# Kernel tuning notes

Hardware: AMD Instinct MI355X
Metric: run time of the kernel (lower is better)

## Reference

```python
import jax, jax.numpy as jnp
import numpy as np

EMBED = 1024
HEAD = 64

def setup_inputs() -> dict:
    key = jax.random.key(0)
    k1, k2, k3, k4 = jax.random.split(key, 4)
    embeddings = jax.random.normal(k1, (8, 2048, EMBED), dtype=jnp.float32)
    # nn.Linear weight is [out, in]; we store transposed [in, out] for x @ W
    scale = 1.0 / np.sqrt(EMBED)
    Wk = jax.random.uniform(k2, (EMBED, HEAD), dtype=jnp.float32, minval=-scale, maxval=scale)
    Wq = jax.random.uniform(k3, (EMBED, HEAD), dtype=jnp.float32, minval=-scale, maxval=scale)
    Wv = jax.random.uniform(k4, (EMBED, HEAD), dtype=jnp.float32, minval=-scale, maxval=scale)
    return {"embeddings": embeddings, "Wq": Wq, "Wk": Wk, "Wv": Wv}

def reference(embeddings, Wq, Wk, Wv):
    B, S, D = embeddings.shape
    q = embeddings @ Wq  # [B,S,H]
    k = embeddings @ Wk
    v = embeddings @ Wv
    norm = k.shape[-1] ** (-0.5)
    scores = jnp.einsum('bqh,bkh->bqk', q, k) * norm  # [B,S,S]
    causal = jnp.tril(jnp.ones((S, S), dtype=bool))
    scores = jnp.where(causal, scores, -jnp.inf)
    weights = jax.nn.softmax(scores, axis=-1)
    # dropout p=0.0 (eval-equivalent): identity
    return jnp.einsum('bqk,bkh->bqh', weights, v)
```

## Files before the change

### kernel.cpp

```cpp
#include <hip/hip_runtime.h>

#define SEQ   2048
#define NBATCH 8
#define EMB   1024
#define HD    64
#define QKVSZ (NBATCH * SEQ * HD)
#define WTSZ  (3 * HD * EMB)
#define PSLOT2 4224

typedef __attribute__((ext_vector_type(8))) short bf16x8;
typedef __attribute__((ext_vector_type(4))) float f32x4;

__device__ inline unsigned short f2b(float f) {
  union { float f; unsigned int i; } u; u.f = f;
  unsigned int r = (u.i + 0x7FFFu + ((u.i >> 16) & 1u)) >> 16;
  return (unsigned short)r;
}

__global__ __launch_bounds__(256) void wtrans_kernel(const float* __restrict__ wq,
                                                     const float* __restrict__ wk,
                                                     const float* __restrict__ wv,
                                                     unsigned short* __restrict__ wt) {
  int i = blockIdx.x * 256 + threadIdx.x;
  int kb  = i / 12288;
  int rem = i - kb * 12288;
  int m   = rem >> 12;
  int c   = (rem >> 6) & 63;
  int kd  = rem & 63;
  const float* src = (m == 0) ? wq : ((m == 1) ? wk : wv);
  int d = kb * 64 + kd;
  wt[i] = f2b(src[d * 64 + c]);
}

#define QKV_ISSUE(kb, pa, pw)                                                       \
  do {                                                                              \
    _Pragma("unroll") for (int j = 0; j < 2; j++) {                                 \
      int u = t + j * 256;                                                          \
      pa[j] = *(const f32x4*)(aBase + (size_t)(u >> 4) * EMB + (kb) * 64 + (u & 15) * 4); \
    }                                                                               \
    _Pragma("unroll") for (int j = 0; j < 3; j++) {                                 \
      int u = t + j * 256;                                                          \
      pw[j] = *(const bf16x8*)(wBase + (size_t)(kb) * 12288 + u * 8);               \
    }                                                                               \
  } while (0)

#define QKV_STAGE(buf, pa, pw)                                                      \
  do {                                                                              \
    _Pragma("unroll") for (int j = 0; j < 2; j++) {                                 \
      int u = t + j * 256;                                                          \
      int row = u >> 4, kq = u & 15;                                                \
      unsigned int lo = (unsigned int)f2b(pa[j][0]) | ((unsigned int)f2b(pa[j][1]) << 16); \
      unsigned int hi = (unsigned int)f2b(pa[j][2]) | ((unsigned int)f2b(pa[j][3]) << 16); \
      uint2 pk; pk.x = lo; pk.y = hi;                                               \
      *(uint2*)((char*)&Ab[buf][0] + row * 128 + ((kq * 8) ^ ((row & 7) << 4))) = pk; \
    }                                                                               \
    _Pragma("unroll") for (int j = 0; j < 3; j++) {                                 \
      int u = t + j * 256;                                                          \
      int coll = u >> 3, kd8 = u & 7;                                               \
      *(bf16x8*)((char*)&Wb[buf][0] + coll * 128 + ((kd8 ^ (coll & 7)) << 4)) = pw[j]; \
    }                                                                               \
  } while (0)

#define QKV_COMPUTE(buf)                                                            \
  do {                                                                              \
    const int arow = wr * 16 + l16;                                                 \
    _Pragma("unroll") for (int kh = 0; kh < 2; kh++) {                              \
      bf16x8 af = *(const bf16x8*)((const char*)&Ab[buf][0] + arow * 128 +          \
                                   ((kh * 64 + quad * 16) ^ ((arow & 7) << 4)));    \
      _Pragma("unroll") for (int j = 0; j < 3; j++) {                               \
        const int coll = (wc * 3 + j) * 16 + l16;                                   \
        bf16x8 wf = *(const bf16x8*)((const char*)&Wb[buf][0] + coll * 128 +        \
                                     ((kh * 64 + quad * 16) ^ ((coll & 7) << 4)));  \
        acc[j] = __builtin_amdgcn_mfma_f32_16x16x32_bf16(af, wf, acc[j], 0, 0, 0);  \
      }                                                                             \
    }                                                                               \
  } while (0)

__global__ __launch_bounds__(256, 4) void qkv_proj_kernel(const float* __restrict__ emb,
                                                          const unsigned short* __restrict__ wt,
                                                          unsigned short* __restrict__ qkv) {
  __shared__ __align__(16) unsigned short Ab[2][32 * 64];
  __shared__ __align__(16) unsigned short Wb[2][96 * 64];

  const int t    = threadIdx.x;
  const int wave = t >> 6;
  const int lane = t & 63;
  const int quad = lane >> 4;
  const int l16  = lane & 15;
  const int bx = blockIdx.x;
  const int rt = bx >> 1;
  const int ch = bx & 1;
  const int wr = wave >> 1;
  const int wc = wave & 1;

  const float* aBase = emb + (size_t)rt * 32 * EMB;
  const unsigned short* wBase = wt + ch * 6144;

  f32x4 acc[3];
#pragma unroll
  for (int j = 0; j < 3; j++) acc[j] = (f32x4){0.f, 0.f, 0.f, 0.f};

  f32x4 paA[2], paB[2];
  bf16x8 pwA[3], pwB[3];

  QKV_ISSUE(0, paA, pwA);
  QKV_ISSUE(1, paB, pwB);
  QKV_STAGE(0, paA, pwA);
  __syncthreads();

#pragma unroll
  for (int k = 0; k < 16; k += 2) {
    if (k + 2 < 16) QKV_ISSUE(k + 2, paA, pwA);
    QKV_COMPUTE(0);
    if (k + 1 < 16) QKV_STAGE(1, paB, pwB);
    __syncthreads();
    if (k + 3 < 16) QKV_ISSUE(k + 3, paB, pwB);
    QKV_COMPUTE(1);
    if (k + 2 < 16) QKV_STAGE(0, paA, pwA);
    __syncthreads();
  }

#pragma unroll
  for (int j = 0; j < 3; j++) {
    int gc = ch * 96 + (wc * 3 + j) * 16 + l16;
    if (gc < 128) {
      int m  = gc >> 6, cm = gc & 63;
#pragma unroll
      for (int r = 0; r < 4; r++) {
        int row = rt * 32 + wr * 16 + quad * 4 + r;
        qkv[(size_t)m * QKVSZ + (size_t)row * HD + cm] = f2b(acc[j][r]);
      }
    }
  }

  if (ch == 1) {
    __syncthreads();
    unsigned short* Vsh = (unsigned short*)&Ab[0][0];
#pragma unroll
    for (int j = 0; j < 3; j++) {
      int gc = 96 + (wc * 3 + j) * 16 + l16;
      if (gc >= 128) {
        int h = gc - 128;
#pragma unroll
        for (int r = 0; r < 4; r++)
          Vsh[h * 40 + wr * 16 + quad * 4 + r] = f2b(acc[j][r]);
      }
    }
    __syncthreads();
    int h  = t >> 2;
    int sq = (t & 3) * 8;
    int row0 = rt * 32;
    int b    = row0 >> 11;
    int seq0 = row0 & 2047;
    bf16x8 vv = *(const bf16x8*)(Vsh + h * 40 + sq);
    *(bf16x8*)(qkv + 2 * (size_t)QKVSZ + ((size_t)(b * 64 + h)) * SEQ + seq0 + sq) = vv;
  }
}

__global__ __launch_bounds__(256, 4) void attn_split(const unsigned short* __restrict__ qkv,
                                                     float* __restrict__ part,
                                                     float* __restrict__ out) {
  __shared__ __align__(16) unsigned short Kb[2][64 * 64];
  __shared__ __align__(16) unsigned short Vb[2][64 * 64];
  __shared__ __align__(16) unsigned short Pb[4][16 * 64];

  const int t    = threadIdx.x;
  const int wave = t >> 6;
  const int lane = t & 63;
  const int quad = lane >> 4;
  const int l16  = lane & 15;
  const int B0 = blockIdx.x;
  const int c  = blockIdx.y;
  const int b  = blockIdx.z;
  const int nch = (B0 >> 2) + 1;
  if (c >= nch) return;
  const int t0 = c * 4;
  const int t1 = min(t0 + 3, B0);
  const int qt = B0 * 4 + wave;
  const int q0 = qt * 16;

  const unsigned short* qg = qkv;
  const unsigned short* kg = qkv + QKVSZ;
  const unsigned short* vg = qkv + 2 * QKVSZ;

  const unsigned short* qptr = qg + ((size_t)(b * SEQ + q0 + l16)) * HD + quad * 8;
  const bf16x8 qf0 = *(const bf16x8*)qptr;
  const bf16x8 qf1 = *(const bf16x8*)(qptr + 32);

  f32x4 o0 = {0,0,0,0}, o1 = {0,0,0,0}, o2 = {0,0,0,0}, o3 = {0,0,0,0};
  float mst[4] = {-INFINITY, -INFINITY, -INFINITY, -INFINITY};
  float lst[4] = {0.f, 0.f, 0.f, 0.f};
  const float sc = 0.125f * 1.44269504088896f;

  bf16x8 kpre[2], vpre[2];
#pragma unroll
  for (int i = 0; i < 2; i++) {
    int u = t + i * 256;
    kpre[i] = *(const bf16x8*)(kg + ((size_t)(b * SEQ + t0 * 64 + (u >> 3))) * HD + (u & 7) * 8);
    vpre[i] = *(const bf16x8*)(vg + ((size_t)(b * 64 + (u >> 3))) * SEQ + t0 * 64 + (u & 7) * 8);
  }
#pragma unroll
  for (int i = 0; i < 2; i++) {
    int u = t + i * 256;
    int row = u >> 3, sb = (u & 7) * 16;
    *(bf16x8*)((char*)&Kb[0][0] + row * 128 + (sb ^ ((row & 7) << 4))) = kpre[i];
    *(bf16x8*)((char*)&Vb[0][0] + row * 128 + (sb ^ ((row & 7) << 4))) = vpre[i];
  }
  __syncthreads();

  for (int kb = t0; kb <= t1; kb++) {
    const int cur = (kb - t0) & 1;

    if (kb < t1) {
#pragma unroll
      for (int i = 0; i < 2; i++) {
        int u = t + i * 256;
        kpre[i] = *(const bf16x8*)(kg + ((size_t)(b * SEQ + (kb + 1) * 64 + (u >> 3))) * HD + (u & 7) * 8);
        vpre[i] = *(const bf16x8*)(vg + ((size_t)(b * 64 + (u >> 3))) * SEQ + (kb + 1) * 64 + (u & 7) * 8);
      }
    }

    f32x4 s[4];
#pragma unroll
    for (int kt = 0; kt < 4; kt++) {
      int row = kt * 16 + l16;
      bf16x8 kf0 = *(const bf16x8*)((char*)&Kb[cur][0] + row * 128 + ((quad * 16) ^ ((row & 7) << 4)));
      bf16x8 kf1 = *(const bf16x8*)((char*)&Kb[cur][0] + row * 128 + ((64 + quad * 16) ^ ((row & 7) << 4)));
      f32x4 z = {0.f, 0.f, 0.f, 0.f};
      z = __builtin_amdgcn_mfma_f32_16x16x32_bf16(qf0, kf0, z, 0, 0, 0);
      z = __builtin_amdgcn_mfma_f32_16x16x32_bf16(qf1, kf1, z, 0, 0, 0);
      s[kt] = z;
    }

    if (kb == B0) {
#pragma unroll
      for (int r = 0; r < 4; r++) {
        int rowg = q0 + quad * 4 + r;
#pragma unroll
        for (int kt = 0; kt < 4; kt++) {
          int col = kb * 64 + kt * 16 + l16;
          float v = s[kt][r] * sc;
          s[kt][r] = (col > rowg) ? -INFINITY : v;
        }
      }
    } else {
#pragma unroll
      for (int r = 0; r < 4; r++)
#pragma unroll
        for (int kt = 0; kt < 4; kt++) s[kt][r] *= sc;
    }

    float alpha[4];
#pragma unroll
    for (int r = 0; r < 4; r++) {
      float mx = fmaxf(fmaxf(s[0][r], s[1][r]), fmaxf(s[2][r], s[3][r]));
#pragma unroll
      for (int off = 1; off < 16; off <<= 1) mx = fmaxf(mx, __shfl_xor(mx, off, 64));
      float mnew = fmaxf(mst[r], mx);
      alpha[r] = exp2f(mst[r] - mnew);
      mst[r] = mnew;
    }
#pragma unroll
    for (int r = 0; r < 4; r++) {
      float sm = 0.f;
#pragma unroll
      for (int kt = 0; kt < 4; kt++) {
        float p = exp2f(s[kt][r] - mst[r]);
        s[kt][r] = p;
        sm += p;
      }
#pragma unroll
      for (int off = 1; off < 16; off <<= 1) sm += __shfl_xor(sm, off, 64);
      lst[r] = lst[r] * alpha[r] + sm;
    }
#pragma unroll
    for (int r = 0; r < 4; r++) { o0[r] *= alpha[r]; o1[r] *= alpha[r]; o2[r] *= alpha[r]; o3[r] *= alpha[r]; }

#pragma unroll
    for (int kt = 0; kt < 4; kt++)
#pragma unroll
      for (int r = 0; r < 4; r++) {
        int row = quad * 4 + r;
        *(unsigned short*)((char*)&Pb[wave][0] + row * 128 +
                           ((kt * 32 + l16 * 2) ^ ((row & 7) << 4))) = f2b(s[kt][r]);
      }

#pragma unroll
    for (int kc = 0; kc < 2; kc++) {
      bf16x8 pf = *(const bf16x8*)((char*)&Pb[wave][0] + l16 * 128 +
                                   ((kc * 64 + quad * 16) ^ ((l16 & 7) << 4)));
      int r0 = l16, r1 = 16 + l16, r2 = 32 + l16, r3 = 48 + l16;
      bf16x8 vf0 = *(const bf16x8*)((char*)&Vb[cur][0] + r0 * 128 + ((kc * 64 + quad * 16) ^ ((r0 & 7) << 4)));
      bf16x8 vf1 = *(const bf16x8*)((char*)&Vb[cur][0] + r1 * 128 + ((kc * 64 + quad * 16) ^ ((r1 & 7) << 4)));
      bf16x8 vf2 = *(const bf16x8*)((char*)&Vb[cur][0] + r2 * 128 + ((kc * 64 + quad * 16) ^ ((r2 & 7) << 4)));
      bf16x8 vf3 = *(const bf16x8*)((char*)&Vb[cur][0] + r3 * 128 + ((kc * 64 + quad * 16) ^ ((r3 & 7) << 4)));
      o0 = __builtin_amdgcn_mfma_f32_16x16x32_bf16(pf, vf0, o0, 0, 0, 0);
      o1 = __builtin_amdgcn_mfma_f32_16x16x32_bf16(pf, vf1, o1, 0, 0, 0);
      o2 = __builtin_amdgcn_mfma_f32_16x16x32_bf16(pf, vf2, o2, 0, 0, 0);
      o3 = __builtin_amdgcn_mfma_f32_16x16x32_bf16(pf, vf3, o3, 0, 0, 0);
    }

    if (kb < t1) {
      const int nb = cur ^ 1;
#pragma unroll
      for (int i = 0; i < 2; i++) {
        int u = t + i * 256;
        int row = u >> 3, sb = (u & 7) * 16;
        *(bf16x8*)((char*)&Kb[nb][0] + row * 128 + (sb ^ ((row & 7) << 4))) = kpre[i];
        *(bf16x8*)((char*)&Vb[nb][0] + row * 128 + (sb ^ ((row & 7) << 4))) = vpre[i];
      }
    }
    __syncthreads();
  }

  if (nch == 1) {
#pragma unroll
    for (int r = 0; r < 4; r++) {
      float inv = 1.f / lst[r];
      int rowg = q0 + quad * 4 + r;
      size_t ob = ((size_t)(b * SEQ + rowg)) * HD + l16;
      out[ob + 0]  = o0[r] * inv;
      out[ob + 16] = o1[r] * inv;
      out[ob + 32] = o2[r] * inv;
      out[ob + 48] = o3[r] * inv;
    }
  } else {
    float* ps = part + ((size_t)((b * 32 + B0) * 8 + c)) * PSLOT2;
#pragma unroll
    for (int r = 0; r < 4; r++) {
      int row = wave * 16 + quad * 4 + r;
      ps[row * 64 + 0  + l16] = o0[r];
      ps[row * 64 + 16 + l16] = o1[r];
      ps[row * 64 + 32 + l16] = o2[r];
      ps[row * 64 + 48 + l16] = o3[r];
      if (l16 == 0) {
        ps[4096 + row] = mst[r];
        ps[4160 + row] = lst[r];
      }
    }
  }
}

__global__ __launch_bounds__(256) void attn_merge(const float* __restrict__ part,
                                                  float* __restrict__ out) {
  const int bx = blockIdx.x;
  const int B0 = 4 + (bx >> 2);
  const int rg = bx & 3;
  const int b  = blockIdx.y;
  const int nch = (B0 >> 2) + 1;
  const int t  = threadIdx.x;
  const int h  = t & 63;
  const int rloc = t >> 6;
  const float* base = part + ((size_t)((b * 32 + B0) * 8)) * PSLOT2;
#pragma unroll
  for (int i = 0; i < 4; i++) {
    int row = rg * 16 + rloc * 4 + i;
    float mv[8], lv[8], ov[8];
#pragma unroll
    for (int cc = 0; cc < 8; cc++) {
      int cs = (cc < nch) ? cc : 0;
      const float* ps = base + (size_t)cs * PSLOT2;
      mv[cc] = ps[4096 + row];
      lv[cc] = ps[4160 + row];
      ov[cc] = ps[row * 64 + h];
    }
    float M = -INFINITY;
#pragma unroll
    for (int cc = 0; cc < 8; cc++) M = fmaxf(M, (cc < nch) ? mv[cc] : -INFINITY);
    float L = 0.f, o = 0.f;
#pragma unroll
    for (int cc = 0; cc < 8; cc++) {
      float e = (cc < nch) ? exp2f(mv[cc] - M) : 0.f;
      L += lv[cc] * e;
      o += ov[cc] * e;
    }
    out[((size_t)(b * SEQ + B0 * 64 + row)) * HD + h] = o / L;
  }
}

extern "C" void kernel_launch(void* const* d_in, const int* in_sizes, int n_in,
                              void* d_out, int out_size, void* d_ws, size_t ws_size,
                              hipStream_t stream) {
  const float* emb = (const float*)d_in[0];
  const float* wq  = (const float*)d_in[1];
  const float* wk  = (const float*)d_in[2];
  const float* wv  = (const float*)d_in[3];
  unsigned short* ws  = (unsigned short*)d_ws;
  unsigned short* wt  = ws;
  unsigned short* qkv = ws + WTSZ;
  float* part = (float*)(ws + WTSZ + 3 * QKVSZ);

  hipLaunchKernelGGL(wtrans_kernel,   dim3(WTSZ / 256), dim3(256), 0, stream, wq, wk, wv, wt);
  hipLaunchKernelGGL(qkv_proj_kernel, dim3(1024),       dim3(256), 0, stream, emb, wt, qkv);
  hipLaunchKernelGGL(attn_split,      dim3(32, 8, 8),   dim3(256), 0, stream, qkv, part, (float*)d_out);
  hipLaunchKernelGGL(attn_merge,      dim3(112, 8),     dim3(256), 0, stream, part, (float*)d_out);
}
```

Before: 159.2 us.

## Load weight and K/V tiles directly into LDS with global_load_lds

Replaces the register-staged global→VGPR→LDS copies of the projection weight tiles and the attention K/V tiles with direct global-to-LDS loads (global_load_lds, 16 bytes per lane). The XOR swizzle is moved to the gather side so each lane fetches from a permuted source address and writes a contiguous LDS slot. The aim is to cut VGPR pressure and the ds_write instructions, letting the double-buffered loads overlap compute. The projection loop also drops from two-deep register prefetch to a single-step pipeline. This relies on the barrier to cover completion of the async LDS writes, with no explicit vmcnt wait, which risks races if the compiler does not insert one.

Result: faster. 155.9 us (-2.1%).

```diff
diff --git a/kernel.cpp b/kernel.cpp
--- a/kernel.cpp
+++ b/kernel.cpp
@@ -16,6 +16,11 @@
   unsigned int r = (u.i + 0x7FFFu + ((u.i >> 16) & 1u)) >> 16;
   return (unsigned short)r;
 }
+
+#define GLOAD_LDS16(g, l)                                              \
+  __builtin_amdgcn_global_load_lds(                                    \
+      (const __attribute__((address_space(1))) void*)(g),              \
+      (__attribute__((address_space(3))) void*)(l), 16, 0, 0)
 
 __global__ __launch_bounds__(256) void wtrans_kernel(const float* __restrict__ wq,
                                                      const float* __restrict__ wk,
@@ -32,19 +37,55 @@
   wt[i] = f2b(src[d * 64 + c]);
 }
 
-#define QKV_ISSUE(kb, pa, pw)                                                       \
+__global__ __launch_bounds__(256, 4) void qkv_proj_kernel(const float* __restrict__ emb,
+                                                          const unsigned short* __restrict__ wt,
+                                                          unsigned short* __restrict__ qkv) {
+  __shared__ __align__(16) unsigned short Ab[2][32 * 64];
+  __shared__ __align__(16) unsigned short Wb[2][96 * 64];
+
+  const int t    = threadIdx.x;
+  const int wave = t >> 6;
+  const int lane = t & 63;
+  const int quad = lane >> 4;
+  const int l16  = lane & 15;
+  const int bx = blockIdx.x;
+  const int rt = bx >> 1;
+  const int ch = bx & 1;
+  const int wr = wave >> 1;
+  const int wc = wave & 1;
+
+  const float* aBase = emb + (size_t)rt * 32 * EMB;
+  const char*  wChunk = (const char*)(wt + ch * 6144);
+
+  int wsrc[3];
+#pragma unroll
+  for (int i = 0; i < 3; i++) {
+    int u = (wave * 3 + i) * 64 + lane;
+    int row = u >> 3, k8 = u & 7;
+    wsrc[i] = row * 128 + ((k8 ^ (row & 7)) << 4);
+  }
+
+  f32x4 acc[3];
+#pragma unroll
+  for (int j = 0; j < 3; j++) acc[j] = (f32x4){0.f, 0.f, 0.f, 0.f};
+  f32x4 pa[2];
+
+#define QKVA_ISSUE(kb)                                                              \
   do {                                                                              \
     _Pragma("unroll") for (int j = 0; j < 2; j++) {                                 \
       int u = t + j * 256;                                                          \
       pa[j] = *(const f32x4*)(aBase + (size_t)(u >> 4) * EMB + (kb) * 64 + (u & 15) * 4); \
     }                                                                               \
-    _Pragma("unroll") for (int j = 0; j < 3; j++) {                                 \
-      int u = t + j * 256;                                                          \
-      pw[j] = *(const bf16x8*)(wBase + (size_t)(kb) * 12288 + u * 8);               \
-    }                                                                               \
   } while (0)
 
-#define QKV_STAGE(buf, pa, pw)                                                      \
+#define QKVW_DMA(kb, buf)                                                           \
+  do {                                                                              \
+    _Pragma("unroll") for (int i = 0; i < 3; i++)                                   \
+      GLOAD_LDS16(wChunk + (size_t)(kb) * 24576 + wsrc[i],                          \
+                  (char*)&Wb[buf][0] + (wave * 3 + i) * 1024);                      \
+  } while (0)
+
+#define QKVA_STAGE(buf)                                                             \
   do {                                                                              \
     _Pragma("unroll") for (int j = 0; j < 2; j++) {                                 \
       int u = t + j * 256;                                                          \
@@ -53,11 +94,6 @@
       unsigned int hi = (unsigned int)f2b(pa[j][2]) | ((unsigned int)f2b(pa[j][3]) << 16); \
       uint2 pk; pk.x = lo; pk.y = hi;                                               \
       *(uint2*)((char*)&Ab[buf][0] + row * 128 + ((kq * 8) ^ ((row & 7) << 4))) = pk; \
-    }                                                                               \
-    _Pragma("unroll") for (int j = 0; j < 3; j++) {                                 \
-      int u = t + j * 256;                                                          \
-      int coll = u >> 3, kd8 = u & 7;                                               \
-      *(bf16x8*)((char*)&Wb[buf][0] + coll * 128 + ((kd8 ^ (coll & 7)) << 4)) = pw[j]; \
     }                                                                               \
   } while (0)
 
@@ -76,47 +112,20 @@
     }                                                                               \
   } while (0)
 
-__global__ __launch_bounds__(256, 4) void qkv_proj_kernel(const float* __restrict__ emb,
-                                                          const unsigned short* __restrict__ wt,
-                                                          unsigned short* __restrict__ qkv) {
-  __shared__ __align__(16) unsigned short Ab[2][32 * 64];
-  __shared__ __align__(16) unsigned short Wb[2][96 * 64];
-
-  const int t    = threadIdx.x;
-  const int wave = t >> 6;
-  const int lane = t & 63;
-  const int quad = lane >> 4;
-  const int l16  = lane & 15;
-  const int bx = blockIdx.x;
-  const int rt = bx >> 1;
-  const int ch = bx & 1;
-  const int wr = wave >> 1;
-  const int wc = wave & 1;
-
-  const float* aBase = emb + (size_t)rt * 32 * EMB;
-  const unsigned short* wBase = wt + ch * 6144;
-
-  f32x4 acc[3];
-#pragma unroll
-  for (int j = 0; j < 3; j++) acc[j] = (f32x4){0.f, 0.f, 0.f, 0.f};
-
-  f32x4 paA[2], paB[2];
-  bf16x8 pwA[3], pwB[3];
-
-  QKV_ISSUE(0, paA, pwA);
-  QKV_ISSUE(1, paB, pwB);
-  QKV_STAGE(0, paA, pwA);
+  QKVA_ISSUE(0);
+  QKVW_DMA(0, 0);
+  QKVA_STAGE(0);
   __syncthreads();
 
-#pragma unroll
-  for (int k = 0; k < 16; k += 2) {
-    if (k + 2 < 16) QKV_ISSUE(k + 2, paA, pwA);
-    QKV_COMPUTE(0);
-    if (k + 1 < 16) QKV_STAGE(1, paB, pwB);
-    __syncthreads();
-    if (k + 3 < 16) QKV_ISSUE(k + 3, paB, pwB);
-    QKV_COMPUTE(1);
-    if (k + 2 < 16) QKV_STAGE(0, paA, pwA);
+  for (int kb = 0; kb < 16; kb++) {
+    const int cur = kb & 1;
+    const int nb  = cur ^ 1;
+    if (kb < 15) {
+      QKVA_ISSUE(kb + 1);
+      QKVW_DMA(kb + 1, nb);
+    }
+    QKV_COMPUTE(cur);
+    if (kb < 15) QKVA_STAGE(nb);
     __syncthreads();
   }
 
@@ -187,36 +196,39 @@
   const bf16x8 qf0 = *(const bf16x8*)qptr;
   const bf16x8 qf1 = *(const bf16x8*)(qptr + 32);
 
+  int koff[2]; size_t voff[2];
+#pragma unroll
+  for (int i = 0; i < 2; i++) {
+    int u = (wave * 2 + i) * 64 + lane;
+    int row = u >> 3, k8 = u & 7;
+    int swz = (k8 ^ (row & 7)) << 4;
+    koff[i] = row * 128 + swz;
+    voff[i] = ((size_t)(b * 64 + row) * SEQ) * 2 + swz;
+  }
+  const char* kgB = (const char*)kg + (size_t)b * SEQ * 128;
+  const char* vgB = (const char*)vg;
+
   f32x4 o0 = {0,0,0,0}, o1 = {0,0,0,0}, o2 = {0,0,0,0}, o3 = {0,0,0,0};
   float mst[4] = {-INFINITY, -INFINITY, -INFINITY, -INFINITY};
   float lst[4] = {0.f, 0.f, 0.f, 0.f};
   const float sc = 0.125f * 1.44269504088896f;
 
-  bf16x8 kpre[2], vpre[2];
 #pragma unroll
   for (int i = 0; i < 2; i++) {
-    int u = t + i * 256;
-    kpre[i] = *(const bf16x8*)(kg + ((size_t)(b * SEQ + t0 * 64 + (u >> 3))) * HD + (u & 7) * 8);
-    vpre[i] = *(const bf16x8*)(vg + ((size_t)(b * 64 + (u >> 3))) * SEQ + t0 * 64 + (u & 7) * 8);
-  }
-#pragma unroll
-  for (int i = 0; i < 2; i++) {
-    int u = t + i * 256;
-    int row = u >> 3, sb = (u & 7) * 16;
-    *(bf16x8*)((char*)&Kb[0][0] + row * 128 + (sb ^ ((row & 7) << 4))) = kpre[i];
-    *(bf16x8*)((char*)&Vb[0][0] + row * 128 + (sb ^ ((row & 7) << 4))) = vpre[i];
+    GLOAD_LDS16(kgB + (size_t)t0 * 8192 + koff[i], (char*)&Kb[0][0] + (wave * 2 + i) * 1024);
+    GLOAD_LDS16(vgB + voff[i] + (size_t)t0 * 128,  (char*)&Vb[0][0] + (wave * 2 + i) * 1024);
   }
   __syncthreads();
 
   for (int kb = t0; kb <= t1; kb++) {
     const int cur = (kb - t0) & 1;
+    const int nb  = cur ^ 1;
 
     if (kb < t1) {
 #pragma unroll
       for (int i = 0; i < 2; i++) {
-        int u = t + i * 256;
-        kpre[i] = *(const bf16x8*)(kg + ((size_t)(b * SEQ + (kb + 1) * 64 + (u >> 3))) * HD + (u & 7) * 8);
-        vpre[i] = *(const bf16x8*)(vg + ((size_t)(b * 64 + (u >> 3))) * SEQ + (kb + 1) * 64 + (u & 7) * 8);
+        GLOAD_LDS16(kgB + (size_t)(kb + 1) * 8192 + koff[i], (char*)&Kb[nb][0] + (wave * 2 + i) * 1024);
+        GLOAD_LDS16(vgB + voff[i] + (size_t)(kb + 1) * 128,  (char*)&Vb[nb][0] + (wave * 2 + i) * 1024);
       }
     }
 
@@ -300,16 +312,6 @@
       o3 = __builtin_amdgcn_mfma_f32_16x16x32_bf16(pf, vf3, o3, 0, 0, 0);
     }
 
-    if (kb < t1) {
-      const int nb = cur ^ 1;
-#pragma unroll
-      for (int i = 0; i < 2; i++) {
-        int u = t + i * 256;
-        int row = u >> 3, sb = (u & 7) * 16;
-        *(bf16x8*)((char*)&Kb[nb][0] + row * 128 + (sb ^ ((row & 7) << 4))) = kpre[i];
-        *(bf16x8*)((char*)&Vb[nb][0] + row * 128 + (sb ^ ((row & 7) << 4))) = vpre[i];
-      }
-    }
     __syncthreads();
   }
 
```
